# Kernel optimization log

Hardware: AMD Instinct MI355X
Metric: run time of the kernel (lower is better)

Reference implementation:

```python
import jax, jax.numpy as jnp
import numpy as np

N_TOK = 384
VOCAB = 50000
N_POS = 52
WDIM = 512
HDIM = 1024
FEAT_DIM = 3 * 16  # np.repeat([len,start,end],16)


def setup_inputs() -> dict:
    key = jax.random.key(0)
    ks = jax.random.split(key, 10)
    s = 0.02  # init scale
    return {
        "sentence": jax.random.randint(ks[0], (N_TOK,), 0, VOCAB),
        "pos_tags": jax.random.randint(ks[1], (N_TOK,), 0, N_POS),
        "We_wrd": jax.random.normal(ks[2], (VOCAB, WDIM), jnp.float32) * s,
        "We_pos": jax.random.normal(ks[3], (N_POS, WDIM), jnp.float32) * s,
        "W_dan1": jax.random.normal(ks[4], (2 * WDIM, HDIM), jnp.float32) * s,
        "b_dan1": jnp.zeros((HDIM,), jnp.float32),
        "W_dan2": jax.random.normal(ks[5], (HDIM, HDIM), jnp.float32) * s,
        "b_dan2": jnp.zeros((HDIM,), jnp.float32),
        "W_s1": jax.random.normal(ks[6], (HDIM + FEAT_DIM, HDIM), jnp.float32) * s,
        "b_s1": jnp.zeros((HDIM,), jnp.float32),
        "W_s2": jax.random.normal(ks[7], (HDIM, 1), jnp.float32) * s,
        "b_s2": jnp.zeros((1,), jnp.float32),
    }


def reference(sentence, pos_tags, We_wrd, We_pos, W_dan1, b_dan1, W_dan2, b_dan2, W_s1, b_s1, W_s2, b_s2):
    n = sentence.shape[0]
    # per-token embedding: concat(pos, word) as in score() with use_pos=True -> [n, 2*wdim]
    emb = jnp.concatenate([We_pos[pos_tags], We_wrd[sentence]], axis=-1)
    # prefix sums so every span mean is O(1): pref[k] = sum of emb[:k]
    pref = jnp.concatenate([jnp.zeros((1, emb.shape[1]), emb.dtype), jnp.cumsum(emb, axis=0)], axis=0)
    # all spans (i, j) with i <= j, as in the double loop over i..n-1, j..n-1
    i_idx, j_idx = np.triu_indices(n)  # static shapes, S = n(n+1)/2
    i_idx = jnp.asarray(i_idx)
    j_idx = jnp.asarray(j_idx)
    end = j_idx + 1
    length = (end - i_idx).astype(emb.dtype)
    # DAN encoder: mean of span embeddings -> 2 relu layers (config['layer']=2)
    mean = (pref[end] - pref[i_idx]) / length[:, None]            # [S, 2*wdim]
    h = jax.nn.relu(mean @ W_dan1 + b_dan1)                        # [S, hdim]
    h = jax.nn.relu(h @ W_dan2 + b_dan2)                           # [S, hdim]
    # phrase feats: np.repeat([len, start, end], 16) -> [S, 48]
    feats = jnp.repeat(jnp.stack([length, i_idx.astype(emb.dtype), end.astype(emb.dtype)], axis=1), 16, axis=1)
    rep = jnp.concatenate([h, feats], axis=1)                      # [S, hdim+48]
    # Wpscore MLP: Linear(ph_dim+48 -> hdim) + relu, Linear(hdim -> 1)
    h2 = jax.nn.relu(rep @ W_s1 + b_s1)
    scores = (h2 @ W_s2 + b_s2)[:, 0]                              # [S]
    return scores
```

## Files before the change

### kernel.cpp

```cpp
#include <hip/hip_runtime.h>

#define NTOK  384
#define SPANS 73920
#define MTILES 584
#define MPAD  (MTILES * 128)
#define HD    1024
#define BK    32
#define KTS   (HD / BK)

typedef unsigned short u16;
typedef __attribute__((ext_vector_type(8))) short short8;
typedef __attribute__((ext_vector_type(4))) float floatx4;

#define VMCNT_IMM(N) (((N) & 0xF) | (((N) >> 4) << 14) | (0x7 << 4) | (0xF << 8))

__device__ __forceinline__ u16 f2bu(float x) {
  union { float f; unsigned u; } un; un.f = x;
  unsigned r = un.u + 0x7fffu + ((un.u >> 16) & 1u);
  return (u16)(r >> 16);
}

__device__ __forceinline__ void gld_lds16(const void* g, void* l) {
  __builtin_amdgcn_global_load_lds(
      (const __attribute__((address_space(1))) void*)g,
      (__attribute__((address_space(3))) void*)l, 16, 0, 0);
}

__global__ void emb_gather(const int* __restrict__ sent, const int* __restrict__ pos,
                           const float* __restrict__ Wwrd, const float* __restrict__ Wpos,
                           u16* __restrict__ embB) {
  int t = blockIdx.x;
  int c = threadIdx.x;
  int pt = pos[t], st = sent[t];
  #pragma unroll
  for (int u = 0; u < 4; ++u) {
    int col = u * 256 + c;
    float v = (col < 512) ? Wpos[(size_t)pt * 512 + col]
                          : Wwrd[(size_t)st * 512 + (col - 512)];
    embB[(size_t)t * HD + col] = f2bu(v);
  }
}

__global__ void prep_spans(int* __restrict__ spI, int* __restrict__ spE, float* __restrict__ spInv,
                           float* __restrict__ scores, const float* __restrict__ bs2) {
  int rf = blockIdx.x * 256 + threadIdx.x;
  if (rf >= MPAD) return;
  int s = rf < SPANS ? rf : SPANS - 1;
  const int n = NTOK;
  double tn = 2.0 * n + 1.0;
  int i = (int)((tn - sqrt(tn * tn - 8.0 * (double)s)) * 0.5);
  if (i < 0) i = 0;
  if (i > n - 1) i = n - 1;
  #define OFF(ii) (((ii) * (2 * n - (ii) + 1)) / 2)
  while (i + 1 <= n - 1 && OFF(i + 1) <= s) ++i;
  while (i > 0 && OFF(i) > s) --i;
  int j = i + (s - OFF(i));
  #undef OFF
  spI[rf] = i;
  spE[rf] = j + 1;
  spInv[rf] = 1.0f / (float)(j + 1 - i);
  if (rf < SPANS) scores[rf] = bs2[0];
}

__global__ void prep_castT(const float* __restrict__ Wd1, const float* __restrict__ Wd2,
                           const float* __restrict__ Ws1,
                           u16* __restrict__ o1, u16* __restrict__ o2, u16* __restrict__ o3) {
  int b = blockIdx.x;
  int w = b >> 10, rem = b & 1023;
  int tk = rem >> 5, tn = rem & 31;
  const float* src = (w == 0) ? Wd1 : ((w == 1) ? Wd2 : Ws1);
  u16* dst = (w == 0) ? o1 : ((w == 1) ? o2 : o3);
  __shared__ u16 tile[32][33];
  int x = threadIdx.x & 31, y = threadIdx.x >> 5;
  int k0 = tk * 32, n0 = tn * 32;
  for (int yy = 0; yy < 32; yy += 8)
    tile[y + yy][x] = f2bu(src[(size_t)(k0 + y + yy) * HD + n0 + x]);
  __syncthreads();
  for (int yy = 0; yy < 32; yy += 8)
    dst[(size_t)(n0 + y + yy) * HD + k0 + x] = tile[x][y + yy];
}

__global__ void prep_svec(const float* __restrict__ Ws1,
                          float* __restrict__ S0, float* __restrict__ S1v, float* __restrict__ S2v) {
  int c = blockIdx.x * 256 + threadIdx.x;
  if (c >= HD) return;
  float a = 0.f, b = 0.f, d = 0.f;
  for (int r = 0; r < 16; ++r) {
    a += Ws1[(size_t)(1024 + r) * HD + c];
    b += Ws1[(size_t)(1040 + r) * HD + c];
    d += Ws1[(size_t)(1056 + r) * HD + c];
  }
  S0[c] = a; S1v[c] = b; S2v[c] = d;
}

__global__ void yscan(const float* __restrict__ Y, float* __restrict__ Qp) {
  __shared__ float buf[NTOK];
  int c = blockIdx.x;
  int t = threadIdx.x;
  buf[t] = Y[(size_t)t * HD + c];
  __syncthreads();
  #pragma unroll
  for (int off = 1; off < NTOK; off <<= 1) {
    float add = (t >= off) ? buf[t - off] : 0.f;
    __syncthreads();
    buf[t] += add;
    __syncthreads();
  }
  if (t == 0) Qp[c] = 0.f;
  Qp[(size_t)(t + 1) * HD + c] = buf[t];
}

__global__ void expand(const float* __restrict__ Qp, const int* __restrict__ spI,
                       const int* __restrict__ spE, const float* __restrict__ spInv,
                       const float* __restrict__ b1, u16* __restrict__ out) {
  int gid = blockIdx.x * 256 + threadIdx.x;
  int row = gid >> 7;
  int c0 = (gid & 127) << 3;
  int i = spI[row], e = spE[row];
  float inv = spInv[row];
  const float* pe = Qp + (size_t)e * HD + c0;
  const float* pi = Qp + (size_t)i * HD + c0;
  const float* bb = b1 + c0;
  u16 tmp[8];
  #pragma unroll
  for (int u = 0; u < 8; ++u) {
    float v = (pe[u] - pi[u]) * inv + bb[u];
    v = v > 0.f ? v : 0.f;
    tmp[u] = f2bu(v);
  }
  *(uint4*)(out + (size_t)row * HD + c0) = *(const uint4*)tmp;
}

template <int EPI>
__global__ __launch_bounds__(256, 3) void gemm_bt(
    const u16* __restrict__ A, const u16* __restrict__ Bt,
    const float* __restrict__ bias, u16* __restrict__ C, float* __restrict__ Cf,
    const int* __restrict__ spI, const int* __restrict__ spE,
    const float* __restrict__ S0, const float* __restrict__ S1v, const float* __restrict__ S2v,
    const float* __restrict__ Ws2, float* __restrict__ scores) {
  __shared__ u16 As[2][128 * BK];
  __shared__ u16 Bs[2][128 * BK];
  int bx = blockIdx.x;
  int mt, nt;
  if (EPI == 2) {
    nt = bx & 7; mt = bx >> 3;
  } else {
    int xcd = bx & 7, k = bx >> 3;
    nt = k & 7;
    mt = xcd + 8 * (k >> 3);
  }
  int m0 = mt * 128, n0 = nt * 128;
  int t = threadIdx.x, lane = t & 63, wid = t >> 6;
  int wm = wid >> 1, wn = wid & 1;
  int q = lane >> 4, r = lane & 15;

  floatx4 acc[4][4] = {};

  int dsub = (lane & 7) ^ ((lane >> 3) & 7);
  int row0 = wid * 16 + 2 * (lane >> 3) + (dsub >> 2);
  int voff = row0 * HD + (dsub & 3) * 8;
  const u16* gA0 = A  + (size_t)m0 * HD;
  const u16* gB0 = Bt + (size_t)n0 * HD;
  int ldsOff0 = wid * 512;
  int ldsOff1 = 2048 + wid * 512;

  auto stage = [&](int kt, int b) {
    const u16* pa = gA0 + voff + kt * BK;
    const u16* pb = gB0 + voff + kt * BK;
    gld_lds16(pa,                   &As[b][ldsOff0]);
    gld_lds16(pa + (size_t)64 * HD, &As[b][ldsOff1]);
    gld_lds16(pb,                   &Bs[b][ldsOff0]);
    gld_lds16(pb + (size_t)64 * HD, &Bs[b][ldsOff1]);
  };

  int oct = (((r & 1) << 2) + q) ^ ((r >> 1) & 7);
  int aoff[4], boff[4];
  #pragma unroll
  for (int x = 0; x < 4; ++x) {
    aoff[x] = (wm * 32 + x * 8 + (r >> 1)) * 64 + oct * 8;
    boff[x] = (wn * 32 + x * 8 + (r >> 1)) * 64 + oct * 8;
  }

  auto compute = [&](int b) {
    short8 af[4];
    #pragma unroll
    for (int x = 0; x < 4; ++x) af[x] = *(const short8*)(&As[b][aoff[x]]);
    #pragma unroll
    for (int ni = 0; ni < 4; ++ni) {
      short8 bf = *(const short8*)(&Bs[b][boff[ni]]);
      #pragma unroll
      for (int mi = 0; mi < 4; ++mi)
        acc[mi][ni] = __builtin_amdgcn_mfma_f32_16x16x32_bf16(af[mi], bf, acc[mi][ni], 0, 0, 0);
    }
  };

  stage(0, 0);
  #pragma unroll 1
  for (int kt = 0; kt < KTS; ++kt) {
    int cur = kt & 1;
    if (kt < KTS - 1) {
      stage(kt + 1, cur ^ 1);
      __builtin_amdgcn_s_waitcnt(VMCNT_IMM(4));
    } else {
      __builtin_amdgcn_s_waitcnt(VMCNT_IMM(0));
    }
    __builtin_amdgcn_s_barrier();
    compute(cur);
    __builtin_amdgcn_s_barrier();
  }

  if (EPI == 2) {
    #pragma unroll
    for (int mi = 0; mi < 4; ++mi) {
      int rowb = m0 + wm * 64 + mi * 16 + q * 4;
      #pragma unroll
      for (int ni = 0; ni < 4; ++ni) {
        int col = n0 + wn * 64 + ni * 16 + r;
        #pragma unroll
        for (int e = 0; e < 4; ++e)
          Cf[(size_t)(rowb + e) * HD + col] = acc[mi][ni][e];
      }
    }
  } else if (EPI == 0) {
    #pragma unroll
    for (int mi = 0; mi < 4; ++mi) {
      int rowb = m0 + wm * 64 + mi * 16 + q * 4;
      #pragma unroll
      for (int ni = 0; ni < 4; ++ni) {
        int col = n0 + wn * 64 + ni * 16 + r;
        float bcol = bias[col];
        #pragma unroll
        for (int e = 0; e < 4; ++e) {
          float v = acc[mi][ni][e] + bcol;
          v = v > 0.f ? v : 0.f;
          C[(size_t)(rowb + e) * HD + col] = f2bu(v);
        }
      }
    }
  } else {
    float bcol[4], s0c[4], s1c[4], s2c[4], wsc[4];
    #pragma unroll
    for (int ni = 0; ni < 4; ++ni) {
      int col = n0 + wn * 64 + ni * 16 + r;
      bcol[ni] = bias[col]; s0c[ni] = S0[col]; s1c[ni] = S1v[col];
      s2c[ni] = S2v[col];  wsc[ni] = Ws2[col];
    }
    #pragma unroll
    for (int mi = 0; mi < 4; ++mi) {
      int rowb = m0 + wm * 64 + mi * 16 + q * 4;
      #pragma unroll
      for (int e = 0; e < 4; ++e) {
        int row = rowb + e;
        float fi = (float)spI[row];
        float fe = (float)spE[row];
        float fl = fe - fi;
        float p = 0.f;
        #pragma unroll
        for (int ni = 0; ni < 4; ++ni) {
          float v = acc[mi][ni][e] + bcol[ni] + fl * s0c[ni] + fi * s1c[ni] + fe * s2c[ni];
          v = v > 0.f ? v : 0.f;
          p += v * wsc[ni];
        }
        p += __shfl_xor(p, 1);
        p += __shfl_xor(p, 2);
        p += __shfl_xor(p, 4);
        p += __shfl_xor(p, 8);
        if (r == 0 && row < SPANS) atomicAdd(&scores[row], p);
      }
    }
  }
}

extern "C" void kernel_launch(void* const* d_in, const int* in_sizes, int n_in,
                              void* d_out, int out_size, void* d_ws, size_t ws_size,
                              hipStream_t stream) {
  const int*   sent = (const int*)d_in[0];
  const int*   pos  = (const int*)d_in[1];
  const float* Wwrd = (const float*)d_in[2];
  const float* Wpos = (const float*)d_in[3];
  const float* Wd1  = (const float*)d_in[4];
  const float* bd1  = (const float*)d_in[5];
  const float* Wd2  = (const float*)d_in[6];
  const float* bd2  = (const float*)d_in[7];
  const float* Ws1  = (const float*)d_in[8];
  const float* bs1  = (const float*)d_in[9];
  const float* Ws2  = (const float*)d_in[10];
  const float* bs2  = (const float*)d_in[11];
  float* scores = (float*)d_out;

  char* w = (char*)d_ws;
  size_t o = 0;
  auto alloc = [&](size_t bytes) {
    char* p = w + o;
    o = (o + bytes + 255) & ~(size_t)255;
    return p;
  };
  int*   spI   = (int*)  alloc((size_t)MPAD * 4);
  int*   spE   = (int*)  alloc((size_t)MPAD * 4);
  float* spInv = (float*)alloc((size_t)MPAD * 4);
  float* S0    = (float*)alloc(4096);
  float* S1v   = (float*)alloc(4096);
  float* S2v   = (float*)alloc(4096);
  u16*   embB  = (u16*)  alloc((size_t)NTOK * HD * 2);
  float* Ybuf  = (float*)alloc((size_t)NTOK * HD * 4);
  float* Qp    = (float*)alloc((size_t)(NTOK + 1) * HD * 4);
  u16* Wd1t = (u16*)alloc((size_t)HD * HD * 2);
  u16* Wd2t = (u16*)alloc((size_t)HD * HD * 2);
  u16* Ws1t = (u16*)alloc((size_t)HD * HD * 2);
  u16* bufA = (u16*)alloc((size_t)MPAD * HD * 2);
  u16* bufB = (u16*)alloc((size_t)MPAD * HD * 2);

  emb_gather<<<NTOK, 256, 0, stream>>>(sent, pos, Wwrd, Wpos, embB);
  prep_spans<<<(MPAD + 255) / 256, 256, 0, stream>>>(spI, spE, spInv, scores, bs2);
  prep_castT<<<3 * 1024, 256, 0, stream>>>(Wd1, Wd2, Ws1, Wd1t, Wd2t, Ws1t);
  prep_svec <<<4, 256, 0, stream>>>(Ws1, S0, S1v, S2v);

  gemm_bt<2><<<(NTOK / 128) * 8, 256, 0, stream>>>(embB, Wd1t, nullptr, nullptr, Ybuf,
                                                   nullptr, nullptr, nullptr, nullptr, nullptr,
                                                   nullptr, nullptr);
  yscan<<<HD, NTOK, 0, stream>>>(Ybuf, Qp);
  expand<<<MPAD / 2, 256, 0, stream>>>(Qp, spI, spE, spInv, bd1, bufA);

  gemm_bt<0><<<MTILES * 8, 256, 0, stream>>>(bufA, Wd2t, bd2, bufB, nullptr,
                                             nullptr, nullptr, nullptr, nullptr, nullptr,
                                             nullptr, nullptr);
  gemm_bt<1><<<MTILES * 8, 256, 0, stream>>>(bufB, Ws1t, bs1, nullptr, nullptr,
                                             spI, spE, S0, S1v, S2v, Ws2, scores);
}
```

Measured before the change: 592.5 us.

## Merge prep kernels, split-K first GEMM, and restructure GEMM main loop pipeline

Folds the four preprocessing kernels into one launch that dispatches on block index. The small first GEMM is split four ways along K into separate Y slices, which yscan sums, so 96 blocks run instead of 24. The GEMM main loop now stages two tiles ahead, preloads fragments into registers and drops one barrier per iteration, aiming to overlap LDS reads with MFMA. This affects the two big GEMMs, which dominate runtime, but the deeper prefetch raises register pressure and the split-K adds extra Y traffic.

```diff
diff --git a/kernel.cpp b/kernel.cpp
--- a/kernel.cpp
+++ b/kernel.cpp
@@ -7,6 +7,7 @@
 #define HD    1024
 #define BK    32
 #define KTS   (HD / BK)
+#define YSLICE ((size_t)NTOK * HD)
 
 typedef unsigned short u16;
 typedef __attribute__((ext_vector_type(8))) short short8;
@@ -26,78 +27,77 @@
       (__attribute__((address_space(3))) void*)l, 16, 0, 0);
 }
 
-__global__ void emb_gather(const int* __restrict__ sent, const int* __restrict__ pos,
-                           const float* __restrict__ Wwrd, const float* __restrict__ Wpos,
-                           u16* __restrict__ embB) {
-  int t = blockIdx.x;
-  int c = threadIdx.x;
-  int pt = pos[t], st = sent[t];
-  #pragma unroll
-  for (int u = 0; u < 4; ++u) {
-    int col = u * 256 + c;
-    float v = (col < 512) ? Wpos[(size_t)pt * 512 + col]
-                          : Wwrd[(size_t)st * 512 + (col - 512)];
-    embB[(size_t)t * HD + col] = f2bu(v);
-  }
-}
-
-__global__ void prep_spans(int* __restrict__ spI, int* __restrict__ spE, float* __restrict__ spInv,
-                           float* __restrict__ scores, const float* __restrict__ bs2) {
-  int rf = blockIdx.x * 256 + threadIdx.x;
-  if (rf >= MPAD) return;
-  int s = rf < SPANS ? rf : SPANS - 1;
-  const int n = NTOK;
-  double tn = 2.0 * n + 1.0;
-  int i = (int)((tn - sqrt(tn * tn - 8.0 * (double)s)) * 0.5);
-  if (i < 0) i = 0;
-  if (i > n - 1) i = n - 1;
-  #define OFF(ii) (((ii) * (2 * n - (ii) + 1)) / 2)
-  while (i + 1 <= n - 1 && OFF(i + 1) <= s) ++i;
-  while (i > 0 && OFF(i) > s) --i;
-  int j = i + (s - OFF(i));
-  #undef OFF
-  spI[rf] = i;
-  spE[rf] = j + 1;
-  spInv[rf] = 1.0f / (float)(j + 1 - i);
-  if (rf < SPANS) scores[rf] = bs2[0];
-}
-
-__global__ void prep_castT(const float* __restrict__ Wd1, const float* __restrict__ Wd2,
-                           const float* __restrict__ Ws1,
-                           u16* __restrict__ o1, u16* __restrict__ o2, u16* __restrict__ o3) {
-  int b = blockIdx.x;
-  int w = b >> 10, rem = b & 1023;
-  int tk = rem >> 5, tn = rem & 31;
-  const float* src = (w == 0) ? Wd1 : ((w == 1) ? Wd2 : Ws1);
-  u16* dst = (w == 0) ? o1 : ((w == 1) ? o2 : o3);
+__global__ void prep_misc(const int* __restrict__ sent, const int* __restrict__ pos,
+                          const float* __restrict__ Wwrd, const float* __restrict__ Wpos,
+                          u16* __restrict__ embB,
+                          int* __restrict__ spI, int* __restrict__ spE, float* __restrict__ spInv,
+                          float* __restrict__ scores, const float* __restrict__ bs2,
+                          const float* __restrict__ Wd1, const float* __restrict__ Wd2,
+                          const float* __restrict__ Ws1,
+                          u16* __restrict__ o1, u16* __restrict__ o2, u16* __restrict__ o3,
+                          float* __restrict__ S0, float* __restrict__ S1v, float* __restrict__ S2v) {
   __shared__ u16 tile[32][33];
-  int x = threadIdx.x & 31, y = threadIdx.x >> 5;
-  int k0 = tk * 32, n0 = tn * 32;
-  for (int yy = 0; yy < 32; yy += 8)
-    tile[y + yy][x] = f2bu(src[(size_t)(k0 + y + yy) * HD + n0 + x]);
-  __syncthreads();
-  for (int yy = 0; yy < 32; yy += 8)
-    dst[(size_t)(n0 + y + yy) * HD + k0 + x] = tile[x][y + yy];
-}
-
-__global__ void prep_svec(const float* __restrict__ Ws1,
-                          float* __restrict__ S0, float* __restrict__ S1v, float* __restrict__ S2v) {
-  int c = blockIdx.x * 256 + threadIdx.x;
-  if (c >= HD) return;
-  float a = 0.f, b = 0.f, d = 0.f;
-  for (int r = 0; r < 16; ++r) {
-    a += Ws1[(size_t)(1024 + r) * HD + c];
-    b += Ws1[(size_t)(1040 + r) * HD + c];
-    d += Ws1[(size_t)(1056 + r) * HD + c];
-  }
-  S0[c] = a; S1v[c] = b; S2v[c] = d;
+  int bx = blockIdx.x;
+  if (bx < 3072) {
+    int w = bx >> 10, rem = bx & 1023;
+    int tk = rem >> 5, tn = rem & 31;
+    const float* src = (w == 0) ? Wd1 : ((w == 1) ? Wd2 : Ws1);
+    u16* dst = (w == 0) ? o1 : ((w == 1) ? o2 : o3);
+    int x = threadIdx.x & 31, y = threadIdx.x >> 5;
+    int k0 = tk * 32, n0 = tn * 32;
+    for (int yy = 0; yy < 32; yy += 8)
+      tile[y + yy][x] = f2bu(src[(size_t)(k0 + y + yy) * HD + n0 + x]);
+    __syncthreads();
+    for (int yy = 0; yy < 32; yy += 8)
+      dst[(size_t)(n0 + y + yy) * HD + k0 + x] = tile[x][y + yy];
+  } else if (bx < 3072 + NTOK) {
+    int t = bx - 3072;
+    int c = threadIdx.x;
+    int pt = pos[t], st = sent[t];
+    #pragma unroll
+    for (int u = 0; u < 4; ++u) {
+      int col = u * 256 + c;
+      float v = (col < 512) ? Wpos[(size_t)pt * 512 + col]
+                            : Wwrd[(size_t)st * 512 + (col - 512)];
+      embB[(size_t)t * HD + col] = f2bu(v);
+    }
+  } else if (bx < 3072 + NTOK + 292) {
+    int rf = (bx - 3072 - NTOK) * 256 + threadIdx.x;
+    if (rf >= MPAD) return;
+    int s = rf < SPANS ? rf : SPANS - 1;
+    const int n = NTOK;
+    double tn2 = 2.0 * n + 1.0;
+    int i = (int)((tn2 - sqrt(tn2 * tn2 - 8.0 * (double)s)) * 0.5);
+    if (i < 0) i = 0;
+    if (i > n - 1) i = n - 1;
+    #define OFF(ii) (((ii) * (2 * n - (ii) + 1)) / 2)
+    while (i + 1 <= n - 1 && OFF(i + 1) <= s) ++i;
+    while (i > 0 && OFF(i) > s) --i;
+    int j = i + (s - OFF(i));
+    #undef OFF
+    spI[rf] = i;
+    spE[rf] = j + 1;
+    spInv[rf] = 1.0f / (float)(j + 1 - i);
+    if (rf < SPANS) scores[rf] = bs2[0];
+  } else {
+    int c = (bx - 3072 - NTOK - 292) * 256 + threadIdx.x;
+    if (c >= HD) return;
+    float a = 0.f, b = 0.f, d = 0.f;
+    for (int r = 0; r < 16; ++r) {
+      a += Ws1[(size_t)(1024 + r) * HD + c];
+      b += Ws1[(size_t)(1040 + r) * HD + c];
+      d += Ws1[(size_t)(1056 + r) * HD + c];
+    }
+    S0[c] = a; S1v[c] = b; S2v[c] = d;
+  }
 }
 
 __global__ void yscan(const float* __restrict__ Y, float* __restrict__ Qp) {
   __shared__ float buf[NTOK];
   int c = blockIdx.x;
   int t = threadIdx.x;
-  buf[t] = Y[(size_t)t * HD + c];
+  size_t idx = (size_t)t * HD + c;
+  buf[t] = Y[idx] + Y[idx + YSLICE] + Y[idx + 2 * YSLICE] + Y[idx + 3 * YSLICE];
   __syncthreads();
   #pragma unroll
   for (int off = 1; off < NTOK; off <<= 1) {
@@ -141,9 +141,11 @@
   __shared__ u16 As[2][128 * BK];
   __shared__ u16 Bs[2][128 * BK];
   int bx = blockIdx.x;
-  int mt, nt;
+  int mt, nt, ks = 0, KT0 = 0, KT1 = KTS;
   if (EPI == 2) {
-    nt = bx & 7; mt = bx >> 3;
+    int rem = bx & 31;
+    nt = rem & 7; ks = rem >> 3; mt = bx >> 5;
+    KT0 = ks * 8; KT1 = KT0 + 8;
   } else {
     int xcd = bx & 7, k = bx >> 3;
     nt = k & 7;
@@ -181,35 +183,38 @@
     boff[x] = (wn * 32 + x * 8 + (r >> 1)) * 64 + oct * 8;
   }
 
-  auto compute = [&](int b) {
-    short8 af[4];
+  short8 af[4], bf[4];
+  auto preload = [&](int b) {
     #pragma unroll
     for (int x = 0; x < 4; ++x) af[x] = *(const short8*)(&As[b][aoff[x]]);
     #pragma unroll
-    for (int ni = 0; ni < 4; ++ni) {
-      short8 bf = *(const short8*)(&Bs[b][boff[ni]]);
+    for (int x = 0; x < 4; ++x) bf[x] = *(const short8*)(&Bs[b][boff[x]]);
+  };
+  auto mfma_burst = [&]() {
+    #pragma unroll
+    for (int ni = 0; ni < 4; ++ni)
       #pragma unroll
       for (int mi = 0; mi < 4; ++mi)
-        acc[mi][ni] = __builtin_amdgcn_mfma_f32_16x16x32_bf16(af[mi], bf, acc[mi][ni], 0, 0, 0);
-    }
+        acc[mi][ni] = __builtin_amdgcn_mfma_f32_16x16x32_bf16(af[mi], bf[ni], acc[mi][ni], 0, 0, 0);
   };
 
-  stage(0, 0);
+  stage(KT0, 0);
+  stage(KT0 + 1, 1);
+  __builtin_amdgcn_s_waitcnt(VMCNT_IMM(4));
+  __builtin_amdgcn_s_barrier();
+  preload(0);
   #pragma unroll 1
-  for (int kt = 0; kt < KTS; ++kt) {
+  for (int kt = KT0; kt < KT1; ++kt) {
     int cur = kt & 1;
-    if (kt < KTS - 1) {
-      stage(kt + 1, cur ^ 1);
-      __builtin_amdgcn_s_waitcnt(VMCNT_IMM(4));
-    } else {
-      __builtin_amdgcn_s_waitcnt(VMCNT_IMM(0));
-    }
+    mfma_burst();
+    __builtin_amdgcn_s_waitcnt(VMCNT_IMM(0));
     __builtin_amdgcn_s_barrier();
-    compute(cur);
-    __builtin_amdgcn_s_barrier();
+    if (kt + 2 < KT1) stage(kt + 2, cur);
+    if (kt + 1 < KT1) preload(cur ^ 1);
   }
 
   if (EPI == 2) {
+    float* Cfk = Cf + (size_t)ks * YSLICE;
     #pragma unroll
     for (int mi = 0; mi < 4; ++mi) {
       int rowb = m0 + wm * 64 + mi * 16 + q * 4;
@@ -218,7 +223,7 @@
         int col = n0 + wn * 64 + ni * 16 + r;
         #pragma unroll
         for (int e = 0; e < 4; ++e)
-          Cf[(size_t)(rowb + e) * HD + col] = acc[mi][ni][e];
+          Cfk[(size_t)(rowb + e) * HD + col] = acc[mi][ni][e];
       }
     }
   } else if (EPI == 0) {
@@ -302,7 +307,7 @@
   float* S1v   = (float*)alloc(4096);
   float* S2v   = (float*)alloc(4096);
   u16*   embB  = (u16*)  alloc((size_t)NTOK * HD * 2);
-  float* Ybuf  = (float*)alloc((size_t)NTOK * HD * 4);
+  float* Ybuf  = (float*)alloc(4 * YSLICE * 4);
   float* Qp    = (float*)alloc((size_t)(NTOK + 1) * HD * 4);
   u16* Wd1t = (u16*)alloc((size_t)HD * HD * 2);
   u16* Wd2t = (u16*)alloc((size_t)HD * HD * 2);
@@ -310,14 +315,15 @@
   u16* bufA = (u16*)alloc((size_t)MPAD * HD * 2);
   u16* bufB = (u16*)alloc((size_t)MPAD * HD * 2);
 
-  emb_gather<<<NTOK, 256, 0, stream>>>(sent, pos, Wwrd, Wpos, embB);
-  prep_spans<<<(MPAD + 255) / 256, 256, 0, stream>>>(spI, spE, spInv, scores, bs2);
-  prep_castT<<<3 * 1024, 256, 0, stream>>>(Wd1, Wd2, Ws1, Wd1t, Wd2t, Ws1t);
-  prep_svec <<<4, 256, 0, stream>>>(Ws1, S0, S1v, S2v);
-
-  gemm_bt<2><<<(NTOK / 128) * 8, 256, 0, stream>>>(embB, Wd1t, nullptr, nullptr, Ybuf,
-                                                   nullptr, nullptr, nullptr, nullptr, nullptr,
-                                                   nullptr, nullptr);
+  prep_misc<<<3072 + NTOK + 292 + 4, 256, 0, stream>>>(
+      sent, pos, Wwrd, Wpos, embB,
+      spI, spE, spInv, scores, bs2,
+      Wd1, Wd2, Ws1, Wd1t, Wd2t, Ws1t,
+      S0, S1v, S2v);
+
+  gemm_bt<2><<<96, 256, 0, stream>>>(embB, Wd1t, nullptr, nullptr, Ybuf,
+                                     nullptr, nullptr, nullptr, nullptr, nullptr,
+                                     nullptr, nullptr);
   yscan<<<HD, NTOK, 0, stream>>>(Ybuf, Qp);
   expand<<<MPAD / 2, 256, 0, stream>>>(Qp, spI, spE, spInv, bd1, bufA);
 
```

Measured after the change: 579.2 us. 1.02x faster.
